# Optimization experiments

Measured on AMD Instinct MI355X. Metric: run time of the kernel, lower is better.

Reference implementation:

```python
import jax, jax.numpy as jnp
import numpy as np

CHANNELS = [4096, 4096, 4096, 4096]
SPARSITY = 0.9  # fraction of weight entries zeroed (sten.random_mask_sparsify frac)
BATCH = 4096


def _sparse_weight(key, out_f, in_f, frac):
    kw, km = jax.random.split(key)
    w = jax.random.normal(kw, (out_f, in_f), dtype=jnp.float32)
    keep = jax.random.uniform(km, (out_f, in_f)) >= frac  # keep ~(1-frac) entries
    return jnp.where(keep, w, 0.0)


def setup_inputs() -> dict:
    key = jax.random.key(0)
    ks = jax.random.split(key, 7)
    x = jax.random.normal(ks[0], (BATCH, CHANNELS[0]), dtype=jnp.float32)
    W1 = _sparse_weight(ks[1], CHANNELS[1], CHANNELS[0], SPARSITY)
    b1 = jax.random.uniform(ks[2], (CHANNELS[1],), dtype=jnp.float32)
    W2 = _sparse_weight(ks[3], CHANNELS[2], CHANNELS[1], SPARSITY)
    b2 = jax.random.uniform(ks[4], (CHANNELS[2],), dtype=jnp.float32)
    W3 = _sparse_weight(ks[5], CHANNELS[3], CHANNELS[2], SPARSITY)
    b3 = jax.random.uniform(ks[6], (CHANNELS[3],), dtype=jnp.float32)
    return {"x": x, "W1": W1, "b1": b1, "W2": W2, "b2": b2, "W3": W3, "b3": b3}


def reference(x, W1, b1, W2, b2, W3, b3):
    # Sequential: Linear -> ReLU -> Linear -> ReLU -> Linear
    # F.linear(x, W, b) == x @ W.T + b; weights already carry the sparsity mask.
    h = x @ W1.T + b1
    h = jax.nn.relu(h)
    h = h @ W2.T + b2
    h = jax.nn.relu(h)
    return h @ W3.T + b3
```

## Files before the change

kernel.cpp:

```cpp
#include <hip/hip_runtime.h>
#include <cstdint>


#define MATN 4096

typedef _Float16 half8 __attribute__((ext_vector_type(8)));
typedef float f32x4 __attribute__((ext_vector_type(4)));

__device__ __forceinline__ void glds16(const void* g, void* l) {
    __builtin_amdgcn_global_load_lds(
        (const __attribute__((address_space(1))) char*)(uintptr_t)g,
        (__attribute__((address_space(3))) char*)(uintptr_t)l,
        16, 0, 0);
}

__device__ __forceinline__ void cvt_body(const float* __restrict__ in,
                                         _Float16* __restrict__ out, int n8) {
    for (int g = blockIdx.x * 256 + threadIdx.x; g < n8; g += gridDim.x * 256) {
        size_t i = (size_t)g * 8;
        float4 a = *(const float4*)(in + i);
        float4 b = *(const float4*)(in + i + 4);
        half8 o;
        o[0] = (_Float16)a.x; o[1] = (_Float16)a.y;
        o[2] = (_Float16)a.z; o[3] = (_Float16)a.w;
        o[4] = (_Float16)b.x; o[5] = (_Float16)b.y;
        o[6] = (_Float16)b.z; o[7] = (_Float16)b.w;
        *(half8*)(out + i) = o;
    }
}

__global__ __launch_bounds__(256)
void cvt_f16(const float* __restrict__ in, _Float16* __restrict__ out, int n8) {
    cvt_body(in, out, n8);
}

__global__ __launch_bounds__(256)
void cvt_f16_2(const float* __restrict__ i0, _Float16* __restrict__ o0,
               const float* __restrict__ i1, _Float16* __restrict__ o1, int n8) {
    cvt_body(blockIdx.y ? i1 : i0, blockIdx.y ? o1 : o0, n8);
}

template <bool RELU, typename OutT>
__global__ __launch_bounds__(256, 4)
void gemm_bt(const _Float16* __restrict__ A, const _Float16* __restrict__ B,
             const float* __restrict__ bias, OutT* __restrict__ C) {
    __shared__ _Float16 sA[128 * 64];
    __shared__ _Float16 sB[128 * 64];

    const int tid  = threadIdx.x;
    const int lane = tid & 63;
    const int w    = tid >> 6;
    const int wm   = w >> 1;
    const int wn   = w & 1;
    const int l16  = lane & 15;
    const int kq   = lane >> 4;

    const int tileM = blockIdx.y * 128;
    const int tileN = blockIdx.x * 128;

    f32x4 acc[4][4] = {};

    const int rin = tid >> 3;
    const int gch = (tid & 7) ^ (rin & 7);
    const _Float16* Ap = A + (size_t)(tileM + rin) * MATN + gch * 8;
    const _Float16* Bp = B + (size_t)(tileN + rin) * MATN + gch * 8;
    const size_t rstep = (size_t)32 * MATN;

    char* sAl = (char*)sA + w * 1024;
    char* sBl = (char*)sB + w * 1024;

    const int sl0 = kq ^ (l16 & 7);
    const int sl1 = sl0 ^ 4;
    const _Float16* rA0 = sA + (wm * 64 + l16) * 64 + sl0 * 8;
    const _Float16* rA1 = sA + (wm * 64 + l16) * 64 + sl1 * 8;
    const _Float16* rB0 = sB + (wn * 64 + l16) * 64 + sl0 * 8;
    const _Float16* rB1 = sB + (wn * 64 + l16) * 64 + sl1 * 8;

    for (int k0 = 0; k0 < MATN; k0 += 64) {
#pragma unroll
        for (int c = 0; c < 4; ++c) glds16(Ap + c * rstep, sAl + c * 4096);
#pragma unroll
        for (int c = 0; c < 4; ++c) glds16(Bp + c * rstep, sBl + c * 4096);
        Ap += 64; Bp += 64;
        __syncthreads();

        half8 af[4], bf[4];
#pragma unroll
        for (int mi = 0; mi < 4; ++mi) af[mi] = *(const half8*)(rA0 + mi * 1024);
#pragma unroll
        for (int ni = 0; ni < 4; ++ni) bf[ni] = *(const half8*)(rB0 + ni * 1024);
#pragma unroll
        for (int mi = 0; mi < 4; ++mi)
#pragma unroll
            for (int ni = 0; ni < 4; ++ni)
                acc[mi][ni] = __builtin_amdgcn_mfma_f32_16x16x32_f16(
                    af[mi], bf[ni], acc[mi][ni], 0, 0, 0);
#pragma unroll
        for (int mi = 0; mi < 4; ++mi) af[mi] = *(const half8*)(rA1 + mi * 1024);
#pragma unroll
        for (int ni = 0; ni < 4; ++ni) bf[ni] = *(const half8*)(rB1 + ni * 1024);
#pragma unroll
        for (int mi = 0; mi < 4; ++mi)
#pragma unroll
            for (int ni = 0; ni < 4; ++ni)
                acc[mi][ni] = __builtin_amdgcn_mfma_f32_16x16x32_f16(
                    af[mi], bf[ni], acc[mi][ni], 0, 0, 0);
        __syncthreads();
    }

#pragma unroll
    for (int ni = 0; ni < 4; ++ni) {
        const int gn = tileN + wn * 64 + ni * 16 + l16;
        const float bv = bias[gn];
#pragma unroll
        for (int mi = 0; mi < 4; ++mi) {
            const int gm = tileM + wm * 64 + mi * 16 + kq * 4;
#pragma unroll
            for (int r = 0; r < 4; ++r) {
                float v = acc[mi][ni][r] + bv;
                if (RELU) v = v > 0.f ? v : 0.f;
                C[(size_t)(gm + r) * MATN + gn] = (OutT)v;
            }
        }
    }
}

extern "C" void kernel_launch(void* const* d_in, const int* in_sizes, int n_in,
                              void* d_out, int out_size, void* d_ws, size_t ws_size,
                              hipStream_t stream) {
    const float* x  = (const float*)d_in[0];
    const float* W1 = (const float*)d_in[1];
    const float* b1 = (const float*)d_in[2];
    const float* W2 = (const float*)d_in[3];
    const float* b2 = (const float*)d_in[4];
    const float* W3 = (const float*)d_in[5];
    const float* b3 = (const float*)d_in[6];
    float* out = (float*)d_out;

    const size_t MAT = (size_t)MATN * MATN;
    _Float16* xb = (_Float16*)d_ws;
    _Float16* wb = (_Float16*)((char*)d_ws + MAT * 2);
    _Float16* h1 = (_Float16*)((char*)d_ws + MAT * 4);
    _Float16* h2 = xb;

    const int n8 = (int)(MAT / 8);
    dim3 ggrid(MATN / 128, MATN / 128);

    cvt_f16_2<<<dim3(2048, 2), 256, 0, stream>>>(x, xb, W1, wb, n8);
    gemm_bt<true, _Float16><<<ggrid, 256, 0, stream>>>(xb, wb, b1, h1);

    cvt_f16<<<2048, 256, 0, stream>>>(W2, wb, n8);
    gemm_bt<true, _Float16><<<ggrid, 256, 0, stream>>>(h1, wb, b2, h2);

    cvt_f16<<<2048, 256, 0, stream>>>(W3, wb, n8);
    gemm_bt<false, float><<<ggrid, 256, 0, stream>>>(h2, wb, b3, out);
}
```

Baseline: 594.7 us.

## Double-buffer LDS tiles to prefetch next K-slice during MFMA compute

```diff
diff --git a/kernel.cpp b/kernel.cpp
--- a/kernel.cpp
+++ b/kernel.cpp
@@ -41,11 +41,11 @@
 }
 
 template <bool RELU, typename OutT>
-__global__ __launch_bounds__(256, 4)
+__global__ __launch_bounds__(256, 2)
 void gemm_bt(const _Float16* __restrict__ A, const _Float16* __restrict__ B,
              const float* __restrict__ bias, OutT* __restrict__ C) {
-    __shared__ _Float16 sA[128 * 64];
-    __shared__ _Float16 sB[128 * 64];
+    __shared__ _Float16 sA[2][128 * 64];
+    __shared__ _Float16 sB[2][128 * 64];
 
     const int tid  = threadIdx.x;
     const int lane = tid & 63;
@@ -66,29 +66,40 @@
     const _Float16* Bp = B + (size_t)(tileN + rin) * MATN + gch * 8;
     const size_t rstep = (size_t)32 * MATN;
 
-    char* sAl = (char*)sA + w * 1024;
-    char* sBl = (char*)sB + w * 1024;
+    const int sl0 = kq ^ (l16 & 7);
+    const int roffA = (wm * 64 + l16) * 64 + sl0 * 8;
+    const int roffB = (wn * 64 + l16) * 64 + sl0 * 8;
+    const int x1 = ((sl0 ^ 4) - sl0) * 8;
 
-    const int sl0 = kq ^ (l16 & 7);
-    const int sl1 = sl0 ^ 4;
-    const _Float16* rA0 = sA + (wm * 64 + l16) * 64 + sl0 * 8;
-    const _Float16* rA1 = sA + (wm * 64 + l16) * 64 + sl1 * 8;
-    const _Float16* rB0 = sB + (wn * 64 + l16) * 64 + sl0 * 8;
-    const _Float16* rB1 = sB + (wn * 64 + l16) * 64 + sl1 * 8;
+    {
+        char* da = (char*)sA[0] + w * 1024;
+        char* db = (char*)sB[0] + w * 1024;
+#pragma unroll
+        for (int c = 0; c < 4; ++c) glds16(Ap + c * rstep, da + c * 4096);
+#pragma unroll
+        for (int c = 0; c < 4; ++c) glds16(Bp + c * rstep, db + c * 4096);
+        Ap += 64; Bp += 64;
+    }
 
-    for (int k0 = 0; k0 < MATN; k0 += 64) {
+    for (int j = 0; j < 64; ++j) {
+        __syncthreads();
+        if (j < 63) {
+            char* da = (char*)sA[(j + 1) & 1] + w * 1024;
+            char* db = (char*)sB[(j + 1) & 1] + w * 1024;
 #pragma unroll
-        for (int c = 0; c < 4; ++c) glds16(Ap + c * rstep, sAl + c * 4096);
+            for (int c = 0; c < 4; ++c) glds16(Ap + c * rstep, da + c * 4096);
 #pragma unroll
-        for (int c = 0; c < 4; ++c) glds16(Bp + c * rstep, sBl + c * 4096);
-        Ap += 64; Bp += 64;
-        __syncthreads();
+            for (int c = 0; c < 4; ++c) glds16(Bp + c * rstep, db + c * 4096);
+            Ap += 64; Bp += 64;
+        }
 
+        const _Float16* cA = sA[j & 1] + roffA;
+        const _Float16* cB = sB[j & 1] + roffB;
         half8 af[4], bf[4];
 #pragma unroll
-        for (int mi = 0; mi < 4; ++mi) af[mi] = *(const half8*)(rA0 + mi * 1024);
+        for (int mi = 0; mi < 4; ++mi) af[mi] = *(const half8*)(cA + mi * 1024);
 #pragma unroll
-        for (int ni = 0; ni < 4; ++ni) bf[ni] = *(const half8*)(rB0 + ni * 1024);
+        for (int ni = 0; ni < 4; ++ni) bf[ni] = *(const half8*)(cB + ni * 1024);
 #pragma unroll
         for (int mi = 0; mi < 4; ++mi)
 #pragma unroll
@@ -96,16 +107,15 @@
                 acc[mi][ni] = __builtin_amdgcn_mfma_f32_16x16x32_f16(
                     af[mi], bf[ni], acc[mi][ni], 0, 0, 0);
 #pragma unroll
-        for (int mi = 0; mi < 4; ++mi) af[mi] = *(const half8*)(rA1 + mi * 1024);
+        for (int mi = 0; mi < 4; ++mi) af[mi] = *(const half8*)(cA + mi * 1024 + x1);
 #pragma unroll
-        for (int ni = 0; ni < 4; ++ni) bf[ni] = *(const half8*)(rB1 + ni * 1024);
+        for (int ni = 0; ni < 4; ++ni) bf[ni] = *(const half8*)(cB + ni * 1024 + x1);
 #pragma unroll
         for (int mi = 0; mi < 4; ++mi)
 #pragma unroll
             for (int ni = 0; ni < 4; ++ni)
                 acc[mi][ni] = __builtin_amdgcn_mfma_f32_16x16x32_f16(
                     af[mi], bf[ni], acc[mi][ni], 0, 0, 0);
-        __syncthreads();
     }
 
 #pragma unroll
```

Measured after the change: 604.0 us. No clear change (+1.6%).
